# Performance work log

Measured on AMD Instinct MI355X. Metric: run time of the kernel, lower is better.

## Reference

```python
import jax, jax.numpy as jnp
import numpy as np

N_NODES = 50000
N_EDGES = 400000
IN_CH = 1024
FEAT_CH = 128
HID = FEAT_CH // 4  # heads=4 -> 32
OUT_CH = 3
BN_EPS = 1e-5
LRELU_SLOPE = 0.01


def setup_inputs() -> dict:
    key = jax.random.key(0)
    ks = jax.random.split(key, 16)
    features = jax.random.normal(ks[0], (N_NODES, IN_CH), dtype=jnp.float32)
    edges = jax.random.randint(ks[1], (2, N_EDGES), 0, N_NODES, dtype=jnp.int64)
    edges2 = jax.random.randint(ks[2], (2, N_EDGES), 0, N_NODES, dtype=jnp.int64)
    edge_features = jax.random.normal(ks[3], (N_EDGES, 1), dtype=jnp.float32)
    additional_feature = jax.random.normal(ks[4], (N_NODES, 20), dtype=jnp.float32)
    # SAGEConv params: lin_l (applied to aggregated neighbors, has bias), lin_r (root, no bias)
    s = 1.0 / np.sqrt(IN_CH)
    W_l = jax.random.uniform(ks[5], (FEAT_CH, IN_CH), jnp.float32, -s, s)
    b_l = jax.random.uniform(ks[6], (FEAT_CH,), jnp.float32, -s, s)
    W_r = jax.random.uniform(ks[7], (FEAT_CH, IN_CH), jnp.float32, -s, s)
    s1 = 1.0 / np.sqrt(FEAT_CH)
    fc1_w = jax.random.uniform(ks[8], (HID, FEAT_CH), jnp.float32, -s1, s1)
    fc1_b = jax.random.uniform(ks[9], (HID,), jnp.float32, -s1, s1)
    s2 = 1.0 / np.sqrt(HID)
    fc2_w = jax.random.uniform(ks[10], (OUT_CH, HID), jnp.float32, -s2, s2)
    fc2_b = jax.random.uniform(ks[11], (OUT_CH,), jnp.float32, -s2, s2)
    bn_gamma = 1.0 + 0.1 * jax.random.normal(ks[12], (HID,), dtype=jnp.float32)
    bn_beta = 0.1 * jax.random.normal(ks[13], (HID,), dtype=jnp.float32)
    bn_mean = 0.1 * jax.random.normal(ks[14], (HID,), dtype=jnp.float32)
    bn_var = jnp.abs(1.0 + 0.1 * jax.random.normal(ks[15], (HID,), dtype=jnp.float32))
    return {
        "features": features, "edges": edges, "edges2": edges2,
        "edge_features": edge_features, "additional_feature": additional_feature,
        "W_l": W_l, "b_l": b_l, "W_r": W_r,
        "fc1_w": fc1_w, "fc1_b": fc1_b, "fc2_w": fc2_w, "fc2_b": fc2_b,
        "bn_gamma": bn_gamma, "bn_beta": bn_beta, "bn_mean": bn_mean, "bn_var": bn_var,
    }


def reference(features, edges, edges2, edge_features, additional_feature,
              W_l, b_l, W_r, fc1_w, fc1_b, fc2_w, fc2_b,
              bn_gamma, bn_beta, bn_mean, bn_var):
    src, dst = edges2[0], edges2[1]  # messages flow src -> dst
    # mean aggregation of neighbor features per target node
    agg = jax.ops.segment_sum(features[src], dst, num_segments=N_NODES)  # [N, in]
    cnt = jax.ops.segment_sum(jnp.ones((src.shape[0],), features.dtype), dst,
                              num_segments=N_NODES)
    mean_agg = agg / jnp.maximum(cnt, 1.0)[:, None]
    # SAGEConv: lin_l(mean_agg) + lin_r(x)
    x = mean_agg @ W_l.T + b_l + features @ W_r.T  # [N, 128]
    x = jax.nn.leaky_relu(x, LRELU_SLOPE)  # dropout: identity in eval
    h = x @ fc1_w.T + fc1_b  # [N, 32]
    h = jax.nn.relu(h)
    # BatchNorm1d (eval mode, running stats)
    h = (h - bn_mean) * jax.lax.rsqrt(bn_var + BN_EPS) * bn_gamma + bn_beta
    return h @ fc2_w.T + fc2_b  # [N, 3]
```

## Files before the change

kernel.cpp:

```cpp
#include <hip/hip_runtime.h>
#include <hip/hip_bf16.h>

#define N_NODES 50000
#define N_EDGES 400000
#define IN_CH 1024
#define FEAT 128
#define HID 32
#define OUT_CH 3

#define GBM 128
#define GBK 64

typedef short bf16x8 __attribute__((ext_vector_type(8)));
typedef float f32x4 __attribute__((ext_vector_type(4)));

static __device__ __forceinline__ unsigned short f2bf(float x) {
  unsigned int u = __float_as_uint(x);
  return (unsigned short)((u + 0x7FFFu + ((u >> 16) & 1u)) >> 16);
}
static __device__ __forceinline__ float bflo(unsigned v) { return __uint_as_float(v << 16); }
static __device__ __forceinline__ float bfhi(unsigned v) { return __uint_as_float(v & 0xFFFF0000u); }

static __device__ __forceinline__ bf16x8 cvt8(const float4 a, const float4 b) {
  __hip_bfloat162 p0 = __float22bfloat162_rn({a.x, a.y});
  __hip_bfloat162 p1 = __float22bfloat162_rn({a.z, a.w});
  __hip_bfloat162 p2 = __float22bfloat162_rn({b.x, b.y});
  __hip_bfloat162 p3 = __float22bfloat162_rn({b.z, b.w});
  bf16x8 u;
  u[0] = *(short*)&p0.x; u[1] = *(short*)&p0.y;
  u[2] = *(short*)&p1.x; u[3] = *(short*)&p1.y;
  u[4] = *(short*)&p2.x; u[5] = *(short*)&p2.y;
  u[6] = *(short*)&p3.x; u[7] = *(short*)&p3.y;
  return u;
}

static __device__ __forceinline__ void gl16(const void* g, void* l) {
  __builtin_amdgcn_global_load_lds(
      (const __attribute__((address_space(1))) unsigned int*)g,
      (__attribute__((address_space(3))) unsigned int*)l, 16, 0, 0);
}

__global__ void convert_w(const float* __restrict__ Wl, const float* __restrict__ Wr,
                          unsigned short* __restrict__ wbf, int* __restrict__ cnt) {
  const int gtid = blockIdx.x * blockDim.x + threadIdx.x;
  const int stride = gridDim.x * blockDim.x;
  for (int i = gtid; i < 2 * FEAT * IN_CH; i += stride) {
    int row = i >> 10;
    float v = (row < FEAT) ? Wl[i] : Wr[i - FEAT * IN_CH];
    wbf[i] = f2bf(v);
  }
  for (int i = gtid; i < N_NODES; i += stride) cnt[i] = 0;
}

__global__ __launch_bounds__(256, 2) void gemm_y(const float* __restrict__ feat,
                                                 const unsigned short* __restrict__ wbf,
                                                 unsigned short* __restrict__ Ybf,
                                                 unsigned short* __restrict__ Yrbf) {
  __shared__ __align__(16) char smem[65536];
  char* aL = smem;
  char* bL = smem + 32768;
  const int t = threadIdx.x;
  const int lane = t & 63;
  const int w = t >> 6;
  const int wm = w >> 1, wn = w & 1;
  const int R0 = blockIdx.x * GBM;

  int goA[8], goB[8];
#pragma unroll
  for (int j = 0; j < 8; ++j) {
    {
      int c16 = j * 256 + t;
      int row = c16 >> 4, cpos = c16 & 15;
      int phys = cpos ^ (row & 15);
      int grow = R0 + row; grow = grow < N_NODES ? grow : N_NODES - 1;
      goA[j] = grow * (IN_CH * 4) + phys * 16;
    }
    {
      int c16 = j * 256 + t;
      int row = c16 >> 3, cpos = c16 & 7;
      int phys = cpos ^ (row & 7);
      goB[j] = row * (IN_CH * 2) + phys * 16;
    }
  }
  const char* featB = (const char*)feat;
  const char* wbfB = (const char*)wbf;

  f32x4 acc[4][8];
#pragma unroll
  for (int m = 0; m < 4; ++m)
#pragma unroll
    for (int n = 0; n < 8; ++n) acc[m][n] = (f32x4){0.f, 0.f, 0.f, 0.f};

  const int r16 = lane & 15, kq = lane >> 4;

  for (int it = 0; it < IN_CH / GBK; ++it) {
    const int K0 = it * GBK;
#pragma unroll
    for (int j = 0; j < 8; ++j)
      gl16(featB + goA[j] + K0 * 4, aL + j * 4096 + w * 1024);
#pragma unroll
    for (int j = 0; j < 8; ++j)
      gl16(wbfB + goB[j] + K0 * 2, bL + j * 4096 + w * 1024);
    __syncthreads();
#pragma unroll
    for (int ks = 0; ks < 2; ++ks) {
      bf16x8 av[4], bv[8];
#pragma unroll
      for (int m = 0; m < 4; ++m) {
        const int row = wm * 64 + m * 16 + r16;
        const int l0 = ks * 8 + kq * 2;
        const int sw = row & 15;
        const float4 lo = *(const float4*)(aL + row * 256 + ((l0) ^ sw) * 16);
        const float4 hi = *(const float4*)(aL + row * 256 + ((l0 + 1) ^ sw) * 16);
        av[m] = cvt8(lo, hi);
      }
#pragma unroll
      for (int n = 0; n < 8; ++n) {
        const int row = wn * 128 + n * 16 + r16;
        const int l = ks * 4 + kq;
        bv[n] = *(const bf16x8*)(bL + row * 128 + ((l) ^ (row & 7)) * 16);
      }
#pragma unroll
      for (int m = 0; m < 4; ++m)
#pragma unroll
        for (int n = 0; n < 8; ++n)
          acc[m][n] = __builtin_amdgcn_mfma_f32_16x16x32_bf16(av[m], bv[n], acc[m][n], 0, 0, 0);
    }
    __syncthreads();
  }

  const int kq4 = lane >> 4;
  unsigned short* dst = (wn == 0) ? Ybf : Yrbf;
#pragma unroll
  for (int m = 0; m < 4; ++m) {
#pragma unroll
    for (int reg = 0; reg < 4; ++reg) {
      int row = R0 + wm * 64 + m * 16 + kq4 * 4 + reg;
      if (row < N_NODES) {
#pragma unroll
        for (int n = 0; n < 8; ++n)
          dst[(size_t)row * FEAT + n * 16 + r16] = f2bf(acc[m][n][reg]);
      }
    }
  }
}

__global__ __launch_bounds__(256) void deg_kernel(const int* __restrict__ e2,
                                                  int* __restrict__ cnt) {
  int e = blockIdx.x * 256 + threadIdx.x;
  if (e < N_EDGES) atomicAdd(&cnt[e2[N_EDGES + e]], 1);
}

static __device__ __forceinline__ int blockScanExcl(int v, int t, int* wsum) {
  int incl = v;
#pragma unroll
  for (int off = 1; off < 64; off <<= 1) {
    int u = __shfl_up(incl, off);
    if ((t & 63) >= off) incl += u;
  }
  const int wid = t >> 6;
  if ((t & 63) == 63) wsum[wid] = incl;
  __syncthreads();
  int base = 0;
#pragma unroll
  for (int k = 0; k < 4; ++k)
    if (k < wid) base += wsum[k];
  return base + incl - v;
}

#define SCAN_B ((N_NODES + 255) / 256)

__global__ __launch_bounds__(256) void scanA(const int* __restrict__ cnt,
                                             int* __restrict__ bsum) {
  __shared__ int lds[4];
  const int t = threadIdx.x;
  const int i = blockIdx.x * 256 + t;
  int v = (i < N_NODES) ? cnt[i] : 0;
  int s = v;
#pragma unroll
  for (int off = 32; off > 0; off >>= 1) s += __shfl_down(s, off);
  if ((t & 63) == 0) lds[t >> 6] = s;
  __syncthreads();
  if (t == 0) bsum[blockIdx.x] = lds[0] + lds[1] + lds[2] + lds[3];
}

__global__ __launch_bounds__(256) void scanB(const int* __restrict__ bsum,
                                             int* __restrict__ boff) {
  __shared__ int wsum[4];
  const int t = threadIdx.x;
  int v = (t < SCAN_B) ? bsum[t] : 0;
  int e = blockScanExcl(v, t, wsum);
  if (t < SCAN_B) boff[t] = e;
}

__global__ __launch_bounds__(256) void scanC(const int* __restrict__ cnt,
                                             const int* __restrict__ boff,
                                             int* __restrict__ rowptr) {
  __shared__ int wsum[4];
  const int t = threadIdx.x;
  const int i = blockIdx.x * 256 + t;
  int v = (i < N_NODES) ? cnt[i] : 0;
  int e = blockScanExcl(v, t, wsum);
  if (i < N_NODES) rowptr[i] = boff[blockIdx.x] + e;
  if (i == 0) rowptr[N_NODES] = N_EDGES;
}

__global__ __launch_bounds__(256) void fill_kernel(const int* __restrict__ e2,
                                                   const int* __restrict__ rowptr,
                                                   int* __restrict__ cur,
                                                   int* __restrict__ csr_src) {
  int e = blockIdx.x * 256 + threadIdx.x;
  if (e < N_EDGES) {
    int src = e2[e];
    int dst = e2[N_EDGES + e];
    int pos = atomicAdd(&cur[dst], -1) - 1;
    csr_src[rowptr[dst] + pos] = src;
  }
}

#define NPB 32
__global__ __launch_bounds__(256) void gather_mlp(
    const int* __restrict__ rowptr, const int* __restrict__ csr_src,
    const unsigned short* __restrict__ Ybf, const unsigned short* __restrict__ Yrbf,
    const float* __restrict__ b_l,
    const float* __restrict__ fc1_w, const float* __restrict__ fc1_b,
    const float* __restrict__ fc2_w, const float* __restrict__ fc2_b,
    const float* __restrict__ gamma, const float* __restrict__ beta,
    const float* __restrict__ mean, const float* __restrict__ var,
    float* __restrict__ out) {
  __shared__ float wT[FEAT * 33];
  __shared__ float xs[4][FEAT];
  __shared__ float hsb[4][HID];
  __shared__ float w2s[OUT_CH * HID];
  const int t = threadIdx.x;
  const int wid = t >> 6, lane = t & 63;

  for (int idx = t; idx < HID * FEAT; idx += 256) {
    int h = idx >> 7, k = idx & 127;
    wT[k * 33 + h] = fc1_w[idx];
  }
  if (t < OUT_CH * HID) w2s[t] = fc2_w[t];
  const int h = lane & 31, half = lane >> 5;
  float bns, bnb, f1bh;
  {
    float g = gamma[h], mu = mean[h], v = var[h], b = beta[h];
    bns = g * rsqrtf(v + 1e-5f);
    bnb = b - mu * bns;
    f1bh = fc1_b[h];
  }
  const float2 bl2 = *(const float2*)(b_l + 2 * lane);
  __syncthreads();

  for (int i = 0; i < 8; ++i) {
    const int n = blockIdx.x * NPB + wid * 8 + i;
    if (n >= N_NODES) break;
    const int start = rowptr[n], end = rowptr[n + 1];
    float a0 = 0.f, a1 = 0.f;
    int j = start;
    for (; j + 3 < end; j += 4) {
      int s0 = csr_src[j], s1 = csr_src[j + 1], s2 = csr_src[j + 2], s3 = csr_src[j + 3];
      unsigned v0 = *(const unsigned*)(Ybf + (size_t)s0 * FEAT + 2 * lane);
      unsigned v1 = *(const unsigned*)(Ybf + (size_t)s1 * FEAT + 2 * lane);
      unsigned v2 = *(const unsigned*)(Ybf + (size_t)s2 * FEAT + 2 * lane);
      unsigned v3 = *(const unsigned*)(Ybf + (size_t)s3 * FEAT + 2 * lane);
      a0 += bflo(v0) + bflo(v1) + bflo(v2) + bflo(v3);
      a1 += bfhi(v0) + bfhi(v1) + bfhi(v2) + bfhi(v3);
    }
    for (; j < end; ++j) {
      unsigned v = *(const unsigned*)(Ybf + (size_t)csr_src[j] * FEAT + 2 * lane);
      a0 += bflo(v);
      a1 += bfhi(v);
    }
    const float rdeg = 1.0f / fmaxf((float)(end - start), 1.0f);
    const unsigned vy = *(const unsigned*)(Yrbf + (size_t)n * FEAT + 2 * lane);
    float x0 = a0 * rdeg + bl2.x + bflo(vy);
    float x1 = a1 * rdeg + bl2.y + bfhi(vy);
    x0 = x0 > 0.f ? x0 : 0.01f * x0;
    x1 = x1 > 0.f ? x1 : 0.01f * x1;
    xs[wid][2 * lane] = x0;
    xs[wid][2 * lane + 1] = x1;
    float p = 0.f;
    const float* xv = xs[wid] + half * 64;
    const float* wv = wT + (half * 64) * 33 + h;
#pragma unroll 16
    for (int k = 0; k < 64; ++k) p += wv[k * 33] * xv[k];
    p += __shfl_xor(p, 32);
    if (half == 0) {
      float a = fmaxf(p + f1bh, 0.f);
      hsb[wid][h] = a * bns + bnb;
    }
    if (lane < OUT_CH) {
      float o = fc2_b[lane];
#pragma unroll
      for (int k2 = 0; k2 < HID; ++k2) o += hsb[wid][k2] * w2s[lane * HID + k2];
      out[n * 3 + lane] = o;
    }
  }
}

extern "C" void kernel_launch(void* const* d_in, const int* in_sizes, int n_in,
                              void* d_out, int out_size, void* d_ws, size_t ws_size,
                              hipStream_t stream) {
  const float* feat = (const float*)d_in[0];
  const int* e2 = (const int*)d_in[2];
  const float* Wl = (const float*)d_in[5];
  const float* bl = (const float*)d_in[6];
  const float* Wr = (const float*)d_in[7];
  const float* f1w = (const float*)d_in[8];
  const float* f1b = (const float*)d_in[9];
  const float* f2w = (const float*)d_in[10];
  const float* f2b = (const float*)d_in[11];
  const float* gma = (const float*)d_in[12];
  const float* bta = (const float*)d_in[13];
  const float* mu = (const float*)d_in[14];
  const float* var = (const float*)d_in[15];
  float* out = (float*)d_out;

  char* ws = (char*)d_ws;
  unsigned short* wbf = (unsigned short*)ws;
  unsigned short* Ybf = (unsigned short*)(ws + 524288);
  unsigned short* Yrbf = (unsigned short*)(ws + 524288 + 12800000);
  size_t off = 524288 + 12800000 + 12800000;
  int* rowptr = (int*)(ws + off);
  off += 200016;
  int* cnt = (int*)(ws + off);
  off += 200000;
  int* csr_src = (int*)(ws + off);
  off += (size_t)N_EDGES * 4;
  int* bsum = (int*)(ws + off);
  off += SCAN_B * 4;
  int* boff = (int*)(ws + off);

  const int EB = (N_EDGES + 255) / 256;
  convert_w<<<256, 256, 0, stream>>>(Wl, Wr, wbf, cnt);
  deg_kernel<<<EB, 256, 0, stream>>>(e2, cnt);
  scanA<<<SCAN_B, 256, 0, stream>>>(cnt, bsum);
  scanB<<<1, 256, 0, stream>>>(bsum, boff);
  scanC<<<SCAN_B, 256, 0, stream>>>(cnt, boff, rowptr);
  fill_kernel<<<EB, 256, 0, stream>>>(e2, rowptr, cnt, csr_src);
  gemm_y<<<(N_NODES + GBM - 1) / GBM, 256, 0, stream>>>(feat, wbf, Ybf, Yrbf);
  gather_mlp<<<(N_NODES + NPB - 1) / NPB, 256, 0, stream>>>(
      rowptr, csr_src, Ybf, Yrbf, bl, f1w, f1b, f2w, f2b, gma, bta, mu, var, out);
}
```

Before: 164.8 us.

## Double-buffer gemm_y LDS tiles with GBK=32 to overlap global loads and MFMA

The feature GEMM halves its K-tile to 32 and splits the 64KB of LDS into two buffers. While MFMAs run on the current tile, the next tile is prefetched with global_load_lds, and partial vmcnt waits plus raw s_barrier replace the two __syncthreads per iteration. This hides global-load latency behind compute. In exchange it doubles the iteration count, so there is more barrier overhead per unit of work, and the hand-written waitcnt/barrier sequence must order LDS writes correctly.

```diff
diff --git a/kernel.cpp b/kernel.cpp
--- a/kernel.cpp
+++ b/kernel.cpp
@@ -9,7 +9,7 @@
 #define OUT_CH 3
 
 #define GBM 128
-#define GBK 64
+#define GBK 32
 
 typedef short bf16x8 __attribute__((ext_vector_type(8)));
 typedef float f32x4 __attribute__((ext_vector_type(4)));
@@ -40,6 +40,9 @@
       (__attribute__((address_space(3))) unsigned int*)l, 16, 0, 0);
 }
 
+#define WAIT_BAR(N) asm volatile("s_waitcnt vmcnt(" #N ")\n\ts_barrier" ::: "memory")
+#define BARRIER() asm volatile("s_barrier" ::: "memory")
+
 __global__ void convert_w(const float* __restrict__ Wl, const float* __restrict__ Wr,
                           unsigned short* __restrict__ wbf, int* __restrict__ cnt) {
   const int gtid = blockIdx.x * blockDim.x + threadIdx.x;
@@ -57,34 +60,42 @@
                                                  unsigned short* __restrict__ Ybf,
                                                  unsigned short* __restrict__ Yrbf) {
   __shared__ __align__(16) char smem[65536];
-  char* aL = smem;
-  char* bL = smem + 32768;
   const int t = threadIdx.x;
   const int lane = t & 63;
   const int w = t >> 6;
   const int wm = w >> 1, wn = w & 1;
   const int R0 = blockIdx.x * GBM;
 
-  int goA[8], goB[8];
-#pragma unroll
-  for (int j = 0; j < 8; ++j) {
-    {
-      int c16 = j * 256 + t;
-      int row = c16 >> 4, cpos = c16 & 15;
-      int phys = cpos ^ (row & 15);
-      int grow = R0 + row; grow = grow < N_NODES ? grow : N_NODES - 1;
-      goA[j] = grow * (IN_CH * 4) + phys * 16;
-    }
+  int goA[4], goB[4];
+#pragma unroll
+  for (int j = 0; j < 4; ++j) {
     {
       int c16 = j * 256 + t;
       int row = c16 >> 3, cpos = c16 & 7;
       int phys = cpos ^ (row & 7);
+      int grow = R0 + row; grow = grow < N_NODES ? grow : N_NODES - 1;
+      goA[j] = grow * (IN_CH * 4) + phys * 16;
+    }
+    {
+      int c16 = j * 256 + t;
+      int row = c16 >> 2, cpos = c16 & 3;
+      int phys = cpos ^ (row & 3);
       goB[j] = row * (IN_CH * 2) + phys * 16;
     }
   }
   const char* featB = (const char*)feat;
   const char* wbfB = (const char*)wbf;
 
+#define STAGE(K0, buf)                                                     \
+  {                                                                        \
+    char* aD = smem + (buf) * 32768;                                       \
+    char* bD = aD + 16384;                                                 \
+    _Pragma("unroll") for (int j = 0; j < 4; ++j)                          \
+      gl16(featB + goA[j] + (K0) * 4, aD + j * 4096 + w * 1024);           \
+    _Pragma("unroll") for (int j = 0; j < 4; ++j)                          \
+      gl16(wbfB + goB[j] + (K0) * 2, bD + j * 4096 + w * 1024);            \
+  }
+
   f32x4 acc[4][8];
 #pragma unroll
   for (int m = 0; m < 4; ++m)
@@ -92,42 +103,42 @@
     for (int n = 0; n < 8; ++n) acc[m][n] = (f32x4){0.f, 0.f, 0.f, 0.f};
 
   const int r16 = lane & 15, kq = lane >> 4;
-
-  for (int it = 0; it < IN_CH / GBK; ++it) {
-    const int K0 = it * GBK;
-#pragma unroll
-    for (int j = 0; j < 8; ++j)
-      gl16(featB + goA[j] + K0 * 4, aL + j * 4096 + w * 1024);
-#pragma unroll
-    for (int j = 0; j < 8; ++j)
-      gl16(wbfB + goB[j] + K0 * 2, bL + j * 4096 + w * 1024);
-    __syncthreads();
-#pragma unroll
-    for (int ks = 0; ks < 2; ++ks) {
-      bf16x8 av[4], bv[8];
-#pragma unroll
-      for (int m = 0; m < 4; ++m) {
-        const int row = wm * 64 + m * 16 + r16;
-        const int l0 = ks * 8 + kq * 2;
-        const int sw = row & 15;
-        const float4 lo = *(const float4*)(aL + row * 256 + ((l0) ^ sw) * 16);
-        const float4 hi = *(const float4*)(aL + row * 256 + ((l0 + 1) ^ sw) * 16);
-        av[m] = cvt8(lo, hi);
-      }
-#pragma unroll
-      for (int n = 0; n < 8; ++n) {
-        const int row = wn * 128 + n * 16 + r16;
-        const int l = ks * 4 + kq;
-        bv[n] = *(const bf16x8*)(bL + row * 128 + ((l) ^ (row & 7)) * 16);
-      }
-#pragma unroll
-      for (int m = 0; m < 4; ++m)
-#pragma unroll
-        for (int n = 0; n < 8; ++n)
-          acc[m][n] = __builtin_amdgcn_mfma_f32_16x16x32_bf16(av[m], bv[n], acc[m][n], 0, 0, 0);
-    }
-    __syncthreads();
-  }
+  const int NIT = IN_CH / GBK;
+
+  STAGE(0, 0);
+
+  for (int it = 0; it < NIT; ++it) {
+    const int cur = it & 1;
+    char* aC = smem + cur * 32768;
+    char* bC = aC + 16384;
+    if (it + 1 < NIT) {
+      STAGE((it + 1) * GBK, cur ^ 1);
+      WAIT_BAR(8);
+    } else {
+      WAIT_BAR(0);
+    }
+    bf16x8 av[4], bv[8];
+#pragma unroll
+    for (int m = 0; m < 4; ++m) {
+      const int row = wm * 64 + m * 16 + r16;
+      const int sw = row & 7;
+      const float4 lo = *(const float4*)(aC + row * 128 + ((kq * 2) ^ sw) * 16);
+      const float4 hi = *(const float4*)(aC + row * 128 + ((kq * 2 + 1) ^ sw) * 16);
+      av[m] = cvt8(lo, hi);
+    }
+#pragma unroll
+    for (int n = 0; n < 8; ++n) {
+      const int row = wn * 128 + n * 16 + r16;
+      bv[n] = *(const bf16x8*)(bC + row * 64 + (kq ^ (row & 3)) * 16);
+    }
+#pragma unroll
+    for (int m = 0; m < 4; ++m)
+#pragma unroll
+      for (int n = 0; n < 8; ++n)
+        acc[m][n] = __builtin_amdgcn_mfma_f32_16x16x32_bf16(av[m], bv[n], acc[m][n], 0, 0, 0);
+    BARRIER();
+  }
+#undef STAGE
 
   const int kq4 = lane >> 4;
   unsigned short* dst = (wn == 0) ? Ybf : Yrbf;
```

After: 168.1 us. +2.0%, slower.
